# Optimization experiments

Hardware: AMD Instinct MI355X
Metric: run time of the kernel (lower is better)

The kernel has to match this reference:

```python
import jax, jax.numpy as jnp
import numpy as np

B = 64          # batch of graphs
N_GOALS = 16
N_SHELVES = 112
N = N_GOALS + N_SHELVES   # 128 nodes per graph
L = 5           # num_layers
D = 32          # node_embedding_dim
DE = 32         # edge_embedding_dim
DT = 32         # timestep_embedding_dim
D_MSG_IN = 2 * D + DT + 1  # 97


def setup_inputs() -> dict:
    key = jax.random.key(0)
    ks = iter(jax.random.split(key, 40))
    def nrm(shape, s=0.05):
        return jax.random.normal(next(ks), shape, jnp.float32) * s
    inp = {}
    inp["pos"] = jax.random.uniform(next(ks), (B, N_SHELVES, 2), jnp.float32, -1.0, 1.0)
    inp["timesteps"] = jax.random.randint(next(ks), (B,), 0, 1000)
    inp["goal_pos"] = jax.random.uniform(next(ks), (N_GOALS, 2), jnp.float32, -1.0, 1.0)
    inp["W_hin"] = nrm((2, D));            inp["b_hin"] = nrm((D,))
    inp["W_msg1"] = nrm((L, D_MSG_IN, DE)); inp["b_msg1"] = nrm((L, DE))
    inp["W_msg2"] = nrm((L, DE, DE));       inp["b_msg2"] = nrm((L, DE))
    inp["W_att"] = nrm((L, DE, 1));         inp["b_att"] = nrm((L, 1))
    inp["W_pos1"] = nrm((L, DE, DE));       inp["b_pos1"] = nrm((L, DE))
    inp["W_pos2"] = nrm((L, DE, 1));        inp["b_pos2"] = nrm((L, 1))
    inp["W_node1"] = nrm((L - 1, DE + D, D)); inp["b_node1"] = nrm((L - 1, D))
    inp["W_node2"] = nrm((L - 1, D, D));      inp["b_node2"] = nrm((L - 1, D))
    inp["W_t"] = nrm((L - 1, DT, DT));        inp["b_t"] = nrm((L - 1, DT))
    return inp


def _forward(pos, timesteps, goal_pos, W_hin, b_hin, W_msg1, b_msg1, W_msg2, b_msg2,
             W_att, b_att, W_pos1, b_pos1, W_pos2, b_pos2,
             W_node1, b_node1, W_node2, b_node2, W_t, b_t):
    silu = jax.nn.silu
    b = pos.shape[0]
    n_g = goal_pos.shape[0]
    n_sh = pos.shape[1]
    n = n_g + n_sh
    num_layers = W_msg1.shape[0]

    # fully-connected edge template per graph (PyG: edge_index[0]=src=row, edge_index[1]=dst=col)
    src_l = jnp.repeat(jnp.arange(n), n)
    dst_l = jnp.tile(jnp.arange(n), n)
    offs = (jnp.arange(b) * n)[:, None]
    src = (offs + src_l[None, :]).reshape(-1)   # [b*n*n]
    dst = (offs + dst_l[None, :]).reshape(-1)
    e_batch = jnp.repeat(jnp.arange(b), n * n)  # batch[edge_index[0]]

    # node one-hot features: goals [1,0], shelves [0,1]
    h0 = jnp.concatenate([
        jnp.tile(jnp.array([1.0, 0.0], jnp.float32), (n_g, 1)),
        jnp.tile(jnp.array([0.0, 1.0], jnp.float32), (n_sh, 1)),
    ], axis=0)                                   # [n, 2]
    x = jnp.tile(h0, (b, 1))                     # [b*n, 2]

    # node positions: goal positions (shared template) then shelf positions
    p = jnp.concatenate([jnp.broadcast_to(goal_pos, (b, n_g, 2)), pos], axis=1).reshape(-1, 2)

    # sinusoidal timestep embedding
    dt = b_t.shape[-1]
    half = dt // 2
    freqs = jnp.exp(-jnp.log(10000.0) * jnp.arange(half, dtype=jnp.float32) / half)
    ang = timesteps.astype(jnp.float32)[:, None] * freqs[None, :]
    temb = jnp.concatenate([jnp.cos(ang), jnp.sin(ang)], axis=-1)  # [b, dt]

    h = x @ W_hin + b_hin  # [b*n, D]

    for i in range(num_layers):
        te = temb[e_batch]                       # [E, dt]
        pd = p[dst] - p[src]                     # pos_i - pos_j
        radial = jnp.sum(pd * pd, axis=-1, keepdims=True)
        pd = pd / (jax.lax.stop_gradient(jnp.sqrt(radial)) + 1e-6)
        m = jnp.concatenate([h[dst], h[src], radial, te], axis=-1)  # [E, 97]
        m = silu(m @ W_msg1[i] + b_msg1[i])
        m = silu(m @ W_msg2[i] + b_msg2[i])
        m = m * jax.nn.sigmoid(m @ W_att[i] + b_att[i])             # attention gate
        pw = silu(m @ W_pos1[i] + b_pos1[i]) @ W_pos2[i] + b_pos2[i]  # [E, 1]
        aggr_h = jax.ops.segment_sum(m, dst, num_segments=b * n)    # scatter-add
        # scatter-mean: every node receives exactly n incoming edges (fully connected incl. self-loop)
        aggr_p = jax.ops.segment_sum(pd * pw, dst, num_segments=b * n) / n
        if i < num_layers - 1:
            u = silu(jnp.concatenate([h, aggr_h], axis=-1) @ W_node1[i] + b_node1[i])
            u = u @ W_node2[i] + b_node2[i]
            h = jnp.where(u > 0, u, 0.01 * u) + h   # LeakyReLU + residual
            temb = silu(temb @ W_t[i] + b_t[i])
        p = aggr_p + p

    return p.reshape(b, n, 2)[:, n_g:, :].reshape(pos.shape)


def reference(pos, timesteps, goal_pos, W_hin, b_hin, W_msg1, b_msg1, W_msg2, b_msg2,
              W_att, b_att, W_pos1, b_pos1, W_pos2, b_pos2,
              W_node1, b_node1, W_node2, b_node2, W_t, b_t):
    return _forward(pos, timesteps, goal_pos, W_hin, b_hin, W_msg1, b_msg1, W_msg2, b_msg2,
                    W_att, b_att, W_pos1, b_pos1, W_pos2, b_pos2,
                    W_node1, b_node1, W_node2, b_node2, W_t, b_t)
```

## Files before the change

### kernel.cpp

```cpp
#include <hip/hip_runtime.h>
#include <hip/hip_bf16.h>

constexpr int B = 64;
constexpr int NG = 16;
constexpr int NSH = 112;
constexpr int N = 128;
constexpr int NN = B * N;
constexpr int L = 5;

constexpr int OFF_H     = 0;
constexpr int OFF_P0    = OFF_H + NN * 32;
constexpr int OFF_P1    = OFF_P0 + NN * 2;
constexpr int OFF_TEMB0 = OFF_P1 + NN * 2;
constexpr int OFF_TEMB1 = OFF_TEMB0 + B * 32;
constexpr int OFF_HA0   = OFF_TEMB1 + B * 32;
constexpr int OFF_HA1   = OFF_HA0 + NN * 32;
constexpr int OFF_HB0   = OFF_HA1 + NN * 32;
constexpr int OFF_HB1   = OFF_HB0 + NN * 16;

typedef __attribute__((ext_vector_type(8))) short bf16x8;
typedef __attribute__((ext_vector_type(4))) float f32x4;

__device__ __forceinline__ float fsigmoid(float x) {
    return __builtin_amdgcn_rcpf(1.0f + __expf(-x));
}
__device__ __forceinline__ float fsilu(float x) { return x * fsigmoid(x); }
__device__ __forceinline__ short f2bfs(float f) {
    union { __hip_bfloat16 b; short s; } u; u.b = __float2bfloat16(f); return u.s;
}
__device__ __forceinline__ float bf2f(unsigned short u) {
    union { unsigned int i; float f; } v; v.i = ((unsigned int)u) << 16; return v.f;
}
__device__ __forceinline__ unsigned int pk_trunc(float lo, float hi) {
    union { float f; unsigned int u; } a, b;
    a.f = hi; b.f = lo;
    return __builtin_amdgcn_perm(a.u, b.u, 0x07060302u);
}

__global__ __launch_bounds__(256) void setup_pre_kernel(
    float* __restrict__ ws,
    const float* __restrict__ pos, const int* __restrict__ tsteps,
    const float* __restrict__ goal_pos,
    const float* __restrict__ W_hin, const float* __restrict__ b_hin,
    const float* __restrict__ W_msg1, const float* __restrict__ b_msg1)
{
    __shared__ float sT[32];
    const int t = threadIdx.x, bx = blockIdx.x;
    const int tid = bx * 256 + t;
    const int c = tid & 31, node = tid >> 5, g = node >> 7, local = node & 127;
    const int row = (local < NG) ? 0 : 1;

    if (t < 32) {
        const float tf = (float)tsteps[g];
        const int jj = (t < 16) ? t : (t - 16);
        const float ang = tf * expf(-logf(10000.0f) * (float)jj / 16.0f);
        sT[t] = (t < 16) ? cosf(ang) : sinf(ang);
    }
    __syncthreads();
    if ((bx & 15) == 0 && t < 32) ws[OFF_TEMB0 + g * 32 + t] = sT[t];

    ws[OFF_H + tid] = W_hin[row * 32 + c] + b_hin[c];

    if (tid < NN * 2) {
        const int d = tid & 1, nd = tid >> 1, g0 = nd >> 7, loc = nd & 127;
        ws[OFF_P0 + tid] = (loc < NG) ? goal_pos[loc * 2 + d]
                                      : pos[(g0 * NSH + (loc - NG)) * 2 + d];
    }

    const float* __restrict__ W1 = W_msg1;
    float accA = b_msg1[c], accB = 0.f;
#pragma unroll
    for (int k = 0; k < 32; ++k) {
        const float hk = W_hin[row * 32 + k] + b_hin[k];
        accA += hk * W1[k * 32 + c];
        accB += hk * W1[(32 + k) * 32 + c];
    }
#pragma unroll
    for (int k = 0; k < 32; ++k)
        accA += sT[k] * W1[(65 + k) * 32 + c];
    ws[OFF_HA0 + tid] = accA;
    ((unsigned short*)(ws + OFF_HB0))[tid] = (unsigned short)f2bfs(accB);
}

__global__ __attribute__((amdgpu_flat_work_group_size(256, 256)))
__attribute__((amdgpu_waves_per_eu(2, 4))) void edge_kernel(
    float* __restrict__ ws,
    const float* __restrict__ W_msg1, const float* __restrict__ b_msg1,
    const float* __restrict__ W_msg2, const float* __restrict__ b_msg2,
    const float* __restrict__ W_att, const float* __restrict__ b_att,
    const float* __restrict__ W_pos1, const float* __restrict__ b_pos1,
    const float* __restrict__ W_pos2, const float* __restrict__ b_pos2,
    const float* __restrict__ W_node1, const float* __restrict__ b_node1,
    const float* __restrict__ W_node2, const float* __restrict__ b_node2,
    const float* __restrict__ W_t, const float* __restrict__ b_t,
    float* __restrict__ out, int l)
{
    __shared__ unsigned short sHBh[128 * 40];
    __shared__ float sPx[128], sPy[128];
    __shared__ __align__(16) unsigned char uraw[14336];
    __shared__ float sAgg[16][36];
    __shared__ float2 sAgp[16];

    unsigned int* mbuf = (unsigned int*)uraw;
    float2* spn = (float2*)(uraw + 10240);
    float (*sH)[36] = (float(*)[36])uraw;
    unsigned int* nmb = (unsigned int*)(uraw + 2304);

    const int t = threadIdx.x;
    const int bx = blockIdx.x;
    const int g = bx >> 4, qp = bx & 15;
    const int gbase = g << 7;
    const int par = l & 1, op = (l + 1) & 1;

    const float* __restrict__ HAin = ws + (par ? OFF_HA1 : OFF_HA0);
    const unsigned short* __restrict__ HBin = (const unsigned short*)(ws + (par ? OFF_HB1 : OFF_HB0));
    const float* __restrict__ Pin = ws + (par ? OFF_P1 : OFF_P0);

#pragma unroll
    for (int ch = 0; ch < 2; ++ch) {
        const int chunk = t + (ch << 8);
        const int row = chunk >> 2, g4 = chunk & 3;
        *(uint4*)(sHBh + row * 40 + (g4 << 3)) =
            *(const uint4*)(HBin + (gbase + row) * 32 + (g4 << 3));
    }
    if (t < 128) {
        sPx[t] = Pin[(gbase + t) * 2];
        sPy[t] = Pin[(gbase + t) * 2 + 1];
    }
    __syncthreads();

    const int lane = t & 63, w = t >> 6;
    const int c = lane & 15, rg = lane >> 4, kk = rg << 3;

    const float* __restrict__ Wm2L = W_msg2 + l * 1024;
    const float* __restrict__ Wp1L = W_pos1 + l * 1024;
    bf16x8 WB1c0, WB1c1, WBpc0, WBpc1, WBac;
#pragma unroll
    for (int j = 0; j < 8; ++j) {
        WB1c0[j] = f2bfs(Wm2L[(kk + j) * 32 + c]);
        WB1c1[j] = f2bfs(Wm2L[(kk + j) * 32 + c + 16]);
        const int pk = ((kk + j) & 1) * 16 + ((kk + j) >> 1);
        WBpc0[j] = f2bfs(Wp1L[pk * 32 + c]);
        WBpc1[j] = f2bfs(Wp1L[pk * 32 + c + 16]);
        WBac[j]  = f2bfs(W_att[l * 32 + pk]);
    }
    float vwr[8];
    {
        const float* wrR = W_msg1 + l * 97 * 32 + 64 * 32 + kk;
#pragma unroll
        for (int j = 0; j < 8; ++j) vwr[j] = wrR[j];
    }
    const float batt  = b_att[l];
    const float vbm20 = b_msg2[l * 32 + c], vbm21 = b_msg2[l * 32 + c + 16];
    const float vbp10 = b_pos1[l * 32 + c], vbp11 = b_pos1[l * 32 + c + 16];
    const float vwp20 = W_pos2[l * 32 + c], vwp21 = W_pos2[l * 32 + c + 16];
    const float bp2   = b_pos2[l];

    unsigned int* mbA = mbuf + w * 320;
    unsigned int* mbB = mbuf + (w + 4) * 320;

    const int dlA = w, dlB = w + 4;
    const int dlocA = (qp << 3) + dlA, dlocB = (qp << 3) + dlB;
    float vhaA[8], vhaB[8];
    {
        const float* haRA = HAin + (gbase + dlocA) * 32 + kk;
        const float* haRB = HAin + (gbase + dlocB) * 32 + kk;
#pragma unroll
        for (int j = 0; j < 8; ++j) { vhaA[j] = haRA[j]; vhaB[j] = haRB[j]; }
    }
    const float pxdA = sPx[dlocA], pydA = sPy[dlocA];
    const float pxdB = sPx[dlocB], pydB = sPy[dlocB];

    float aghc0A = 0.f, aghc1A = 0.f, apxA = 0.f, apyA = 0.f, spnxA = 0.f, spnyA = 0.f;
    float aghc0B = 0.f, aghc1B = 0.f, apxB = 0.f, apyB = 0.f, spnxB = 0.f, spnyB = 0.f;

#pragma unroll 1
    for (int half = 0; half < 2; ++half) {
        const int src = (half << 6) + lane;
        const float sx = sPx[src], sy = sPy[src];
        const float dxA = pxdA - sx, dyA = pydA - sy;
        const float dxB = pxdB - sx, dyB = pydB - sy;
        const float radialA = dxA * dxA + dyA * dyA;
        const float radialB = dxB * dxB + dyB * dyB;
        const float invA = __builtin_amdgcn_rcpf(__builtin_amdgcn_sqrtf(radialA) + 1e-6f);
        const float invB = __builtin_amdgcn_rcpf(__builtin_amdgcn_sqrtf(radialB) + 1e-6f);
        const float pnxA = dxA * invA, pnyA = dyA * invA;
        const float pnxB = dxB * invB, pnyB = dyB * invB;
        spnxA += pnxA; spnyA += pnyA;
        spnxB += pnxB; spnyB += pnyB;
        spn[w * 64 + lane]       = (float2){pnxA, pnyA};
        spn[(w + 4) * 64 + lane] = (float2){pnxB, pnyB};

#pragma unroll
        for (int tt = 0; tt < 4; ++tt) {
            const float rad_tA = __shfl(radialA, c + (tt << 4));
            const float rad_tB = __shfl(radialB, c + (tt << 4));
            uint4 hraw = *(const uint4*)(sHBh + ((half << 6) + c + (tt << 4)) * 40 + kk);
            const unsigned short* hs = (const unsigned short*)&hraw;
            float xA[8], xB[8];
#pragma unroll
            for (int j = 0; j < 8; ++j) {
                const float hb = bf2f(hs[j]);
                xA[j] = fsilu(vhaA[j] + hb + rad_tA * vwr[j]);
                xB[j] = fsilu(vhaB[j] + hb + rad_tB * vwr[j]);
            }
            union { unsigned int u[4]; bf16x8 v; } afA, afB;
#pragma unroll
            for (int d = 0; d < 4; ++d) {
                afA.u[d] = pk_trunc(xA[2 * d], xA[2 * d + 1]);
                afB.u[d] = pk_trunc(xB[2 * d], xB[2 * d + 1]);
            }
            f32x4 a0A = (f32x4){vbm20, vbm20, vbm20, vbm20};
            f32x4 a1A = (f32x4){vbm21, vbm21, vbm21, vbm21};
            f32x4 a0B = a0A, a1B = a1A;
            a0A = __builtin_amdgcn_mfma_f32_16x16x32_bf16(afA.v, WB1c0, a0A, 0, 0, 0);
            a1A = __builtin_amdgcn_mfma_f32_16x16x32_bf16(afA.v, WB1c1, a1A, 0, 0, 0);
            a0B = __builtin_amdgcn_mfma_f32_16x16x32_bf16(afB.v, WB1c0, a0B, 0, 0, 0);
            a1B = __builtin_amdgcn_mfma_f32_16x16x32_bf16(afB.v, WB1c1, a1B, 0, 0, 0);

            float s0A[4], s1A[4], s0B[4], s1B[4];
#pragma unroll
            for (int j = 0; j < 4; ++j) {
                s0A[j] = fsilu(a0A[j]);
                s1A[j] = fsilu(a1A[j]);
                s0B[j] = fsilu(a0B[j]);
                s1B[j] = fsilu(a1B[j]);
                mbA[((rg << 2) + j) * 20 + c] = pk_trunc(s0A[j], s1A[j]);
                mbB[((rg << 2) + j) * 20 + c] = pk_trunc(s0B[j], s1B[j]);
            }

            union { uint4 u; bf16x8 v; } qaA, qaB;
            qaA.u = *(const uint4*)(mbA + c * 20 + (rg << 2));
            qaB.u = *(const uint4*)(mbB + c * 20 + (rg << 2));
            f32x4 zaA = (f32x4){batt, batt, batt, batt};
            f32x4 zaB = zaA;
            f32x4 z0A = (f32x4){0.f, 0.f, 0.f, 0.f};
            f32x4 z1A = z0A, z0B = z0A, z1B = z0A;
            zaA = __builtin_amdgcn_mfma_f32_16x16x32_bf16(qaA.v, WBac,  zaA, 0, 0, 0);
            z0A = __builtin_amdgcn_mfma_f32_16x16x32_bf16(qaA.v, WBpc0, z0A, 0, 0, 0);
            z1A = __builtin_amdgcn_mfma_f32_16x16x32_bf16(qaA.v, WBpc1, z1A, 0, 0, 0);
            zaB = __builtin_amdgcn_mfma_f32_16x16x32_bf16(qaB.v, WBac,  zaB, 0, 0, 0);
            z0B = __builtin_amdgcn_mfma_f32_16x16x32_bf16(qaB.v, WBpc0, z0B, 0, 0, 0);
            z1B = __builtin_amdgcn_mfma_f32_16x16x32_bf16(qaB.v, WBpc1, z1B, 0, 0, 0);
#pragma unroll
            for (int j = 0; j < 4; ++j) {
                const float attA = fsigmoid(zaA[j]);
                const float attB = fsigmoid(zaB[j]);
                aghc0A += attA * s0A[j];
                aghc1A += attA * s1A[j];
                aghc0B += attB * s0B[j];
                aghc1B += attB * s1B[j];
                const float q0A = fsilu(attA * z0A[j] + vbp10);
                const float q1A = fsilu(attA * z1A[j] + vbp11);
                const float q0B = fsilu(attB * z0B[j] + vbp10);
                const float q1B = fsilu(attB * z1B[j] + vbp11);
                const float pwpA = q0A * vwp20 + q1A * vwp21;
                const float pwpB = q0B * vwp20 + q1B * vwp21;
                const float2 pnA = spn[w * 64 + (tt << 4) + (rg << 2) + j];
                const float2 pnB = spn[(w + 4) * 64 + (tt << 4) + (rg << 2) + j];
                apxA += pwpA * pnA.x;
                apyA += pwpA * pnA.y;
                apxB += pwpB * pnB.x;
                apyB += pwpB * pnB.y;
            }
        }
    }

    aghc0A += __shfl_xor(aghc0A, 16); aghc0A += __shfl_xor(aghc0A, 32);
    aghc1A += __shfl_xor(aghc1A, 16); aghc1A += __shfl_xor(aghc1A, 32);
    aghc0B += __shfl_xor(aghc0B, 16); aghc0B += __shfl_xor(aghc0B, 32);
    aghc1B += __shfl_xor(aghc1B, 16); aghc1B += __shfl_xor(aghc1B, 32);
#pragma unroll
    for (int off = 1; off < 64; off <<= 1) {
        apxA  += __shfl_xor(apxA, off);
        apyA  += __shfl_xor(apyA, off);
        spnxA += __shfl_xor(spnxA, off);
        spnyA += __shfl_xor(spnyA, off);
        apxB  += __shfl_xor(apxB, off);
        apyB  += __shfl_xor(apyB, off);
        spnxB += __shfl_xor(spnxB, off);
        spnyB += __shfl_xor(spnyB, off);
    }
    if (l < L - 1) {
        if (lane < 32) {
            sAgg[dlA][lane] = (lane < 16) ? aghc0A : aghc1A;
            sAgg[dlB][lane] = (lane < 16) ? aghc0B : aghc1B;
        }
        if (lane == 0) {
            sAgp[dlA] = (float2){(apxA + bp2 * spnxA) * (1.0f / 128.0f),
                                 (apyA + bp2 * spnyA) * (1.0f / 128.0f)};
            sAgp[dlB] = (float2){(apxB + bp2 * spnxB) * (1.0f / 128.0f),
                                 (apyB + bp2 * spnyB) * (1.0f / 128.0f)};
        }
    } else if (lane == 0) {
        if (dlocA >= NG) {
            out[(g * NSH + (dlocA - NG)) * 2]     = pxdA + (apxA + bp2 * spnxA) * (1.0f / 128.0f);
            out[(g * NSH + (dlocA - NG)) * 2 + 1] = pydA + (apyA + bp2 * spnyA) * (1.0f / 128.0f);
        }
        if (dlocB >= NG) {
            out[(g * NSH + (dlocB - NG)) * 2]     = pxdB + (apxB + bp2 * spnxB) * (1.0f / 128.0f);
            out[(g * NSH + (dlocB - NG)) * 2 + 1] = pydB + (apyB + bp2 * spnyB) * (1.0f / 128.0f);
        }
    }
    if (l == L - 1) return;

    __syncthreads();

    if (t < 64) {
        const int nbase = bx << 3;
        float* __restrict__ HAout = ws + (op ? OFF_HA1 : OFF_HA0);
        unsigned short* __restrict__ HBout = (unsigned short*)(ws + (op ? OFF_HB1 : OFF_HB0));
        float* __restrict__ Pout = ws + (op ? OFF_P1 : OFF_P0);

        {
            const int row8 = lane >> 3, seg = lane & 7;
            const float* hsrc = ws + OFF_H + (nbase + row8) * 32 + (seg << 2);
#pragma unroll
            for (int j = 0; j < 4; ++j) sH[row8][(seg << 2) + j] = hsrc[j];
        }

        const float* __restrict__ Wn1 = W_node1 + l * 2048;
        const float* __restrict__ Wn2 = W_node2 + l * 1024;
        const float* __restrict__ W1  = W_msg1 + (l + 1) * 97 * 32;
        bf16x8 B1[2][2], B2[2], Ba[2], Bb[2];
#pragma unroll
        for (int j = 0; j < 8; ++j) {
            const int pk = ((kk + j) & 1) * 16 + ((kk + j) >> 1);
#pragma unroll
            for (int nh = 0; nh < 2; ++nh) {
                B1[0][nh][j] = f2bfs(Wn1[(kk + j) * 32 + nh * 16 + c]);
                B1[1][nh][j] = f2bfs(Wn1[(32 + kk + j) * 32 + nh * 16 + c]);
                B2[nh][j]    = f2bfs(Wn2[pk * 32 + nh * 16 + c]);
                Ba[nh][j]    = f2bfs(W1[pk * 32 + nh * 16 + c]);
                Bb[nh][j]    = f2bfs(W1[(32 + pk) * 32 + nh * 16 + c]);
            }
        }

        const int c2 = lane & 31;
        const float* __restrict__ tin = ws + (par ? OFF_TEMB1 : OFF_TEMB0) + g * 32;
        const float* __restrict__ Wt = W_t + l * 1024;
        float a2 = b_t[l * 32 + c2];
#pragma unroll
        for (int k = 0; k < 32; ++k) a2 += tin[k] * Wt[k * 32 + c2];
        const float tnew = fsilu(a2);
        float tv = b_msg1[(l + 1) * 32 + c2];
#pragma unroll
        for (int k = 0; k < 32; ++k) tv += __shfl(tnew, k) * W1[(65 + k) * 32 + c2];
        if ((bx & 15) == 0 && lane < 32)
            ws[(par ? OFF_TEMB0 : OFF_TEMB1) + g * 32 + lane] = tnew;

        union { unsigned int u[4]; bf16x8 v; } A0, A1;
#pragma unroll
        for (int d = 0; d < 4; ++d) {
            A0.u[d] = pk_trunc(sH[c][kk + 2 * d],   sH[c][kk + 2 * d + 1]);
            A1.u[d] = pk_trunc(sAgg[c][kk + 2 * d], sAgg[c][kk + 2 * d + 1]);
        }
        f32x4 u1[2];
#pragma unroll
        for (int nh = 0; nh < 2; ++nh) {
            const float bb = b_node1[l * 32 + nh * 16 + c];
            f32x4 acc = (f32x4){bb, bb, bb, bb};
            acc = __builtin_amdgcn_mfma_f32_16x16x32_bf16(A0.v, B1[0][nh], acc, 0, 0, 0);
            acc = __builtin_amdgcn_mfma_f32_16x16x32_bf16(A1.v, B1[1][nh], acc, 0, 0, 0);
            u1[nh] = acc;
        }

#pragma unroll
        for (int j = 0; j < 4; ++j)
            nmb[((rg << 2) + j) * 20 + c] = pk_trunc(fsilu(u1[0][j]), fsilu(u1[1][j]));
        union { uint4 q; bf16x8 v; } qa;
        qa.q = *(const uint4*)(nmb + c * 20 + (rg << 2));
        f32x4 u2[2];
#pragma unroll
        for (int nh = 0; nh < 2; ++nh) {
            const float bb = b_node2[l * 32 + nh * 16 + c];
            f32x4 acc = (f32x4){bb, bb, bb, bb};
            u2[nh] = __builtin_amdgcn_mfma_f32_16x16x32_bf16(qa.v, B2[nh], acc, 0, 0, 0);
        }

        float hp0[4], hp1[4];
#pragma unroll
        for (int j = 0; j < 4; ++j) {
            const int row = (rg << 2) + j;
            const float h0 = sH[row][c], h1 = sH[row][c + 16];
            const float v0 = u2[0][j], v1 = u2[1][j];
            hp0[j] = (v0 > 0.f ? v0 : 0.01f * v0) + h0;
            hp1[j] = (v1 > 0.f ? v1 : 0.01f * v1) + h1;
            if (row < 8) {
                ws[OFF_H + (nbase + row) * 32 + c]      = hp0[j];
                ws[OFF_H + (nbase + row) * 32 + c + 16] = hp1[j];
            }
            nmb[row * 20 + c] = pk_trunc(hp0[j], hp1[j]);
        }

        qa.q = *(const uint4*)(nmb + c * 20 + (rg << 2));
        f32x4 ha[2], hb[2];
        {
            f32x4 zz = (f32x4){0.f, 0.f, 0.f, 0.f};
#pragma unroll
            for (int nh = 0; nh < 2; ++nh) {
                ha[nh] = __builtin_amdgcn_mfma_f32_16x16x32_bf16(qa.v, Ba[nh], zz, 0, 0, 0);
                hb[nh] = __builtin_amdgcn_mfma_f32_16x16x32_bf16(qa.v, Bb[nh], zz, 0, 0, 0);
            }
        }
        const float tv0 = __shfl(tv, c), tv1 = __shfl(tv, c + 16);
#pragma unroll
        for (int j = 0; j < 4; ++j) {
            const int row = (rg << 2) + j;
            if (row < 8) {
                const int node = nbase + row;
                HAout[node * 32 + c]      = ha[0][j] + tv0;
                HAout[node * 32 + c + 16] = ha[1][j] + tv1;
                HBout[node * 32 + c]      = (unsigned short)f2bfs(hb[0][j]);
                HBout[node * 32 + c + 16] = (unsigned short)f2bfs(hb[1][j]);
            }
        }

        if (lane < 16) {
            const int dl2 = lane >> 1, d = lane & 1;
            const int node = nbase + dl2;
            const float ag = d ? sAgp[dl2].y : sAgp[dl2].x;
            Pout[node * 2 + d] = (par ? ws[OFF_P1 + node * 2 + d]
                                      : ws[OFF_P0 + node * 2 + d]) + ag;
        }
    }
}

extern "C" void kernel_launch(void* const* d_in, const int* in_sizes, int n_in,
                              void* d_out, int out_size, void* d_ws, size_t ws_size,
                              hipStream_t stream)
{
    const float* pos      = (const float*)d_in[0];
    const int*   tsteps   = (const int*)d_in[1];
    const float* goal_pos = (const float*)d_in[2];
    const float* W_hin    = (const float*)d_in[3];
    const float* b_hin    = (const float*)d_in[4];
    const float* W_msg1   = (const float*)d_in[5];
    const float* b_msg1   = (const float*)d_in[6];
    const float* W_msg2   = (const float*)d_in[7];
    const float* b_msg2   = (const float*)d_in[8];
    const float* W_att    = (const float*)d_in[9];
    const float* b_att    = (const float*)d_in[10];
    const float* W_pos1   = (const float*)d_in[11];
    const float* b_pos1   = (const float*)d_in[12];
    const float* W_pos2   = (const float*)d_in[13];
    const float* b_pos2   = (const float*)d_in[14];
    const float* W_node1  = (const float*)d_in[15];
    const float* b_node1  = (const float*)d_in[16];
    const float* W_node2  = (const float*)d_in[17];
    const float* b_node2  = (const float*)d_in[18];
    const float* W_t      = (const float*)d_in[19];
    const float* b_t      = (const float*)d_in[20];

    float* ws = (float*)d_ws;

    setup_pre_kernel<<<1024, 256, 0, stream>>>(ws, pos, tsteps, goal_pos,
                                               W_hin, b_hin, W_msg1, b_msg1);

    for (int l = 0; l < L; ++l)
        edge_kernel<<<1024, 256, 0, stream>>>(ws, W_msg1, b_msg1, W_msg2, b_msg2,
                                              W_att, b_att, W_pos1, b_pos1,
                                              W_pos2, b_pos2, W_node1, b_node1,
                                              W_node2, b_node2, W_t, b_t,
                                              (float*)d_out, l);
}
```

Before: 290.2 us.

## Fuse all message-passing layers into one cooperative persistent kernel with grid sync

Replaces the five per-layer edge_kernel launches with a single cooperative kernel that loops over layers and uses grid.sync between them. Each block handles 16 or 32 destination nodes of one graph instead of the previous 1024-block split. The node update for the next layer is fused into the same block. This removes launch overhead and inter-kernel gaps. In exchange the grid shrinks to 512 or 256 blocks and relies on grid-wide barriers, which may lower parallelism and add barrier cost.

```diff
diff --git a/kernel.cpp b/kernel.cpp
--- a/kernel.cpp
+++ b/kernel.cpp
@@ -1,5 +1,8 @@
 #include <hip/hip_runtime.h>
 #include <hip/hip_bf16.h>
+#include <hip/hip_cooperative_groups.h>
+
+namespace cg = cooperative_groups;
 
 constexpr int B = 64;
 constexpr int NG = 16;
@@ -80,6 +83,367 @@
         accA += sT[k] * W1[(65 + k) * 32 + c];
     ws[OFF_HA0 + tid] = accA;
     ((unsigned short*)(ws + OFF_HB0))[tid] = (unsigned short)f2bfs(accB);
+}
+
+template <int NQP>
+__global__ __attribute__((amdgpu_flat_work_group_size(256, 256)))
+__attribute__((amdgpu_waves_per_eu(2, 4))) void fused_layers_kernel(
+    float* __restrict__ ws,
+    const float* __restrict__ W_msg1, const float* __restrict__ b_msg1,
+    const float* __restrict__ W_msg2, const float* __restrict__ b_msg2,
+    const float* __restrict__ W_att, const float* __restrict__ b_att,
+    const float* __restrict__ W_pos1, const float* __restrict__ b_pos1,
+    const float* __restrict__ W_pos2, const float* __restrict__ b_pos2,
+    const float* __restrict__ W_node1, const float* __restrict__ b_node1,
+    const float* __restrict__ W_node2, const float* __restrict__ b_node2,
+    const float* __restrict__ W_t, const float* __restrict__ b_t,
+    float* __restrict__ out)
+{
+    constexpr int DST  = 128 / NQP;
+    constexpr int SI   = DST / 8;
+    constexpr int BOFF = DST / 2;
+    constexpr int EPP  = DST / 16;
+
+    __shared__ unsigned short sHBh[128 * 40];
+    __shared__ float sPx[128], sPy[128];
+    __shared__ __align__(16) unsigned char uraw[14336];
+    __shared__ float sAgg[32][36];
+    __shared__ float2 sAgp[32];
+
+    unsigned int* mbuf = (unsigned int*)uraw;
+    float2* spn = (float2*)(uraw + 10240);
+    float (*sH)[36] = (float(*)[36])uraw;
+    unsigned int* nmb = (unsigned int*)(uraw + 2304);
+
+    cg::grid_group grid = cg::this_grid();
+
+    const int t = threadIdx.x;
+    const int bx = blockIdx.x;
+    const int g = bx / NQP, qp = bx % NQP;
+    const int gbase = g << 7;
+
+    const int lane = t & 63, w = t >> 6;
+    const int c = lane & 15, rg = lane >> 4, kk = rg << 3;
+
+    unsigned int* mbA = mbuf + w * 320;
+    unsigned int* mbB = mbuf + (w + 4) * 320;
+
+    for (int l = 0; l < L; ++l) {
+        const int par = l & 1, op = par ^ 1;
+
+        const float* __restrict__ HAin = ws + (par ? OFF_HA1 : OFF_HA0);
+        const unsigned short* __restrict__ HBin =
+            (const unsigned short*)(ws + (par ? OFF_HB1 : OFF_HB0));
+        const float* __restrict__ Pin = ws + (par ? OFF_P1 : OFF_P0);
+
+#pragma unroll
+        for (int ch = 0; ch < 2; ++ch) {
+            const int chunk = t + (ch << 8);
+            const int row = chunk >> 2, g4 = chunk & 3;
+            *(uint4*)(sHBh + row * 40 + (g4 << 3)) =
+                *(const uint4*)(HBin + (gbase + row) * 32 + (g4 << 3));
+        }
+        if (t < 128) {
+            sPx[t] = Pin[(gbase + t) * 2];
+            sPy[t] = Pin[(gbase + t) * 2 + 1];
+        }
+        __syncthreads();
+
+        const float* __restrict__ Wm2L = W_msg2 + l * 1024;
+        const float* __restrict__ Wp1L = W_pos1 + l * 1024;
+        bf16x8 WB1c0, WB1c1, WBpc0, WBpc1, WBac;
+#pragma unroll
+        for (int j = 0; j < 8; ++j) {
+            WB1c0[j] = f2bfs(Wm2L[(kk + j) * 32 + c]);
+            WB1c1[j] = f2bfs(Wm2L[(kk + j) * 32 + c + 16]);
+            const int pk = ((kk + j) & 1) * 16 + ((kk + j) >> 1);
+            WBpc0[j] = f2bfs(Wp1L[pk * 32 + c]);
+            WBpc1[j] = f2bfs(Wp1L[pk * 32 + c + 16]);
+            WBac[j]  = f2bfs(W_att[l * 32 + pk]);
+        }
+        float vwr[8];
+        {
+            const float* wrR = W_msg1 + l * 97 * 32 + 64 * 32 + kk;
+#pragma unroll
+            for (int j = 0; j < 8; ++j) vwr[j] = wrR[j];
+        }
+        const float batt  = b_att[l];
+        const float vbm20 = b_msg2[l * 32 + c], vbm21 = b_msg2[l * 32 + c + 16];
+        const float vbp10 = b_pos1[l * 32 + c], vbp11 = b_pos1[l * 32 + c + 16];
+        const float vwp20 = W_pos2[l * 32 + c], vwp21 = W_pos2[l * 32 + c + 16];
+        const float bp2   = b_pos2[l];
+
+#pragma unroll 1
+        for (int si = 0; si < SI; ++si) {
+            const int dlA = (si << 2) + w, dlB = dlA + BOFF;
+            const int dlocA = qp * DST + dlA, dlocB = qp * DST + dlB;
+            float vhaA[8], vhaB[8];
+            {
+                const float* haRA = HAin + (gbase + dlocA) * 32 + kk;
+                const float* haRB = HAin + (gbase + dlocB) * 32 + kk;
+#pragma unroll
+                for (int j = 0; j < 8; ++j) { vhaA[j] = haRA[j]; vhaB[j] = haRB[j]; }
+            }
+            const float pxdA = sPx[dlocA], pydA = sPy[dlocA];
+            const float pxdB = sPx[dlocB], pydB = sPy[dlocB];
+
+            float aghc0A = 0.f, aghc1A = 0.f, apxA = 0.f, apyA = 0.f, spnxA = 0.f, spnyA = 0.f;
+            float aghc0B = 0.f, aghc1B = 0.f, apxB = 0.f, apyB = 0.f, spnxB = 0.f, spnyB = 0.f;
+
+#pragma unroll 1
+            for (int half = 0; half < 2; ++half) {
+                const int src = (half << 6) + lane;
+                const float sx = sPx[src], sy = sPy[src];
+                const float dxA = pxdA - sx, dyA = pydA - sy;
+                const float dxB = pxdB - sx, dyB = pydB - sy;
+                const float radialA = dxA * dxA + dyA * dyA;
+                const float radialB = dxB * dxB + dyB * dyB;
+                const float invA = __builtin_amdgcn_rcpf(__builtin_amdgcn_sqrtf(radialA) + 1e-6f);
+                const float invB = __builtin_amdgcn_rcpf(__builtin_amdgcn_sqrtf(radialB) + 1e-6f);
+                const float pnxA = dxA * invA, pnyA = dyA * invA;
+                const float pnxB = dxB * invB, pnyB = dyB * invB;
+                spnxA += pnxA; spnyA += pnyA;
+                spnxB += pnxB; spnyB += pnyB;
+                spn[w * 64 + lane]       = (float2){pnxA, pnyA};
+                spn[(w + 4) * 64 + lane] = (float2){pnxB, pnyB};
+
+#pragma unroll
+                for (int tt = 0; tt < 4; ++tt) {
+                    const float rad_tA = __shfl(radialA, c + (tt << 4));
+                    const float rad_tB = __shfl(radialB, c + (tt << 4));
+                    uint4 hraw = *(const uint4*)(sHBh + ((half << 6) + c + (tt << 4)) * 40 + kk);
+                    const unsigned short* hs = (const unsigned short*)&hraw;
+                    float xA[8], xB[8];
+#pragma unroll
+                    for (int j = 0; j < 8; ++j) {
+                        const float hb = bf2f(hs[j]);
+                        xA[j] = fsilu(vhaA[j] + hb + rad_tA * vwr[j]);
+                        xB[j] = fsilu(vhaB[j] + hb + rad_tB * vwr[j]);
+                    }
+                    union { unsigned int u[4]; bf16x8 v; } afA, afB;
+#pragma unroll
+                    for (int d = 0; d < 4; ++d) {
+                        afA.u[d] = pk_trunc(xA[2 * d], xA[2 * d + 1]);
+                        afB.u[d] = pk_trunc(xB[2 * d], xB[2 * d + 1]);
+                    }
+                    f32x4 a0A = (f32x4){vbm20, vbm20, vbm20, vbm20};
+                    f32x4 a1A = (f32x4){vbm21, vbm21, vbm21, vbm21};
+                    f32x4 a0B = a0A, a1B = a1A;
+                    a0A = __builtin_amdgcn_mfma_f32_16x16x32_bf16(afA.v, WB1c0, a0A, 0, 0, 0);
+                    a1A = __builtin_amdgcn_mfma_f32_16x16x32_bf16(afA.v, WB1c1, a1A, 0, 0, 0);
+                    a0B = __builtin_amdgcn_mfma_f32_16x16x32_bf16(afB.v, WB1c0, a0B, 0, 0, 0);
+                    a1B = __builtin_amdgcn_mfma_f32_16x16x32_bf16(afB.v, WB1c1, a1B, 0, 0, 0);
+
+                    float s0A[4], s1A[4], s0B[4], s1B[4];
+#pragma unroll
+                    for (int j = 0; j < 4; ++j) {
+                        s0A[j] = fsilu(a0A[j]);
+                        s1A[j] = fsilu(a1A[j]);
+                        s0B[j] = fsilu(a0B[j]);
+                        s1B[j] = fsilu(a1B[j]);
+                        mbA[((rg << 2) + j) * 20 + c] = pk_trunc(s0A[j], s1A[j]);
+                        mbB[((rg << 2) + j) * 20 + c] = pk_trunc(s0B[j], s1B[j]);
+                    }
+
+                    union { uint4 u; bf16x8 v; } qaA, qaB;
+                    qaA.u = *(const uint4*)(mbA + c * 20 + (rg << 2));
+                    qaB.u = *(const uint4*)(mbB + c * 20 + (rg << 2));
+                    f32x4 zaA = (f32x4){batt, batt, batt, batt};
+                    f32x4 zaB = zaA;
+                    f32x4 z0A = (f32x4){0.f, 0.f, 0.f, 0.f};
+                    f32x4 z1A = z0A, z0B = z0A, z1B = z0A;
+                    zaA = __builtin_amdgcn_mfma_f32_16x16x32_bf16(qaA.v, WBac,  zaA, 0, 0, 0);
+                    z0A = __builtin_amdgcn_mfma_f32_16x16x32_bf16(qaA.v, WBpc0, z0A, 0, 0, 0);
+                    z1A = __builtin_amdgcn_mfma_f32_16x16x32_bf16(qaA.v, WBpc1, z1A, 0, 0, 0);
+                    zaB = __builtin_amdgcn_mfma_f32_16x16x32_bf16(qaB.v, WBac,  zaB, 0, 0, 0);
+                    z0B = __builtin_amdgcn_mfma_f32_16x16x32_bf16(qaB.v, WBpc0, z0B, 0, 0, 0);
+                    z1B = __builtin_amdgcn_mfma_f32_16x16x32_bf16(qaB.v, WBpc1, z1B, 0, 0, 0);
+#pragma unroll
+                    for (int j = 0; j < 4; ++j) {
+                        const float attA = fsigmoid(zaA[j]);
+                        const float attB = fsigmoid(zaB[j]);
+                        aghc0A += attA * s0A[j];
+                        aghc1A += attA * s1A[j];
+                        aghc0B += attB * s0B[j];
+                        aghc1B += attB * s1B[j];
+                        const float q0A = fsilu(attA * z0A[j] + vbp10);
+                        const float q1A = fsilu(attA * z1A[j] + vbp11);
+                        const float q0B = fsilu(attB * z0B[j] + vbp10);
+                        const float q1B = fsilu(attB * z1B[j] + vbp11);
+                        const float pwpA = q0A * vwp20 + q1A * vwp21;
+                        const float pwpB = q0B * vwp20 + q1B * vwp21;
+                        const float2 pnA = spn[w * 64 + (tt << 4) + (rg << 2) + j];
+                        const float2 pnB = spn[(w + 4) * 64 + (tt << 4) + (rg << 2) + j];
+                        apxA += pwpA * pnA.x;
+                        apyA += pwpA * pnA.y;
+                        apxB += pwpB * pnB.x;
+                        apyB += pwpB * pnB.y;
+                    }
+                }
+            }
+
+            aghc0A += __shfl_xor(aghc0A, 16); aghc0A += __shfl_xor(aghc0A, 32);
+            aghc1A += __shfl_xor(aghc1A, 16); aghc1A += __shfl_xor(aghc1A, 32);
+            aghc0B += __shfl_xor(aghc0B, 16); aghc0B += __shfl_xor(aghc0B, 32);
+            aghc1B += __shfl_xor(aghc1B, 16); aghc1B += __shfl_xor(aghc1B, 32);
+#pragma unroll
+            for (int off = 1; off < 64; off <<= 1) {
+                apxA  += __shfl_xor(apxA, off);
+                apyA  += __shfl_xor(apyA, off);
+                spnxA += __shfl_xor(spnxA, off);
+                spnyA += __shfl_xor(spnyA, off);
+                apxB  += __shfl_xor(apxB, off);
+                apyB  += __shfl_xor(apyB, off);
+                spnxB += __shfl_xor(spnxB, off);
+                spnyB += __shfl_xor(spnyB, off);
+            }
+            if (l < L - 1) {
+                if (lane < 32) {
+                    sAgg[dlA][lane] = (lane < 16) ? aghc0A : aghc1A;
+                    sAgg[dlB][lane] = (lane < 16) ? aghc0B : aghc1B;
+                }
+                if (lane == 0) {
+                    sAgp[dlA] = (float2){(apxA + bp2 * spnxA) * (1.0f / 128.0f),
+                                         (apyA + bp2 * spnyA) * (1.0f / 128.0f)};
+                    sAgp[dlB] = (float2){(apxB + bp2 * spnxB) * (1.0f / 128.0f),
+                                         (apyB + bp2 * spnyB) * (1.0f / 128.0f)};
+                }
+            } else if (lane == 0) {
+                if (dlocA >= NG) {
+                    out[(g * NSH + (dlocA - NG)) * 2]     = pxdA + (apxA + bp2 * spnxA) * (1.0f / 128.0f);
+                    out[(g * NSH + (dlocA - NG)) * 2 + 1] = pydA + (apyA + bp2 * spnyA) * (1.0f / 128.0f);
+                }
+                if (dlocB >= NG) {
+                    out[(g * NSH + (dlocB - NG)) * 2]     = pxdB + (apxB + bp2 * spnxB) * (1.0f / 128.0f);
+                    out[(g * NSH + (dlocB - NG)) * 2 + 1] = pydB + (apyB + bp2 * spnyB) * (1.0f / 128.0f);
+                }
+            }
+        }
+        if (l == L - 1) break;
+
+        __syncthreads();
+
+        if (t < 64) {
+            float* __restrict__ HAout = ws + (op ? OFF_HA1 : OFF_HA0);
+            unsigned short* __restrict__ HBout = (unsigned short*)(ws + (op ? OFF_HB1 : OFF_HB0));
+            float* __restrict__ Pout = ws + (op ? OFF_P1 : OFF_P0);
+
+            const float* __restrict__ Wn1 = W_node1 + l * 2048;
+            const float* __restrict__ Wn2 = W_node2 + l * 1024;
+            const float* __restrict__ W1n = W_msg1 + (l + 1) * 97 * 32;
+            bf16x8 B1[2][2], B2[2], Ba[2], Bb[2];
+#pragma unroll
+            for (int j = 0; j < 8; ++j) {
+                const int pk = ((kk + j) & 1) * 16 + ((kk + j) >> 1);
+#pragma unroll
+                for (int nh = 0; nh < 2; ++nh) {
+                    B1[0][nh][j] = f2bfs(Wn1[(kk + j) * 32 + nh * 16 + c]);
+                    B1[1][nh][j] = f2bfs(Wn1[(32 + kk + j) * 32 + nh * 16 + c]);
+                    B2[nh][j]    = f2bfs(Wn2[pk * 32 + nh * 16 + c]);
+                    Ba[nh][j]    = f2bfs(W1n[pk * 32 + nh * 16 + c]);
+                    Bb[nh][j]    = f2bfs(W1n[(32 + pk) * 32 + nh * 16 + c]);
+                }
+            }
+
+            const int c2 = lane & 31;
+            const float* __restrict__ tin = ws + (par ? OFF_TEMB1 : OFF_TEMB0) + g * 32;
+            const float* __restrict__ Wt = W_t + l * 1024;
+            float a2 = b_t[l * 32 + c2];
+#pragma unroll
+            for (int k = 0; k < 32; ++k) a2 += tin[k] * Wt[k * 32 + c2];
+            const float tnew = fsilu(a2);
+            float tv = b_msg1[(l + 1) * 32 + c2];
+#pragma unroll
+            for (int k = 0; k < 32; ++k) tv += __shfl(tnew, k) * W1n[(65 + k) * 32 + c2];
+            if (qp == 0 && lane < 32)
+                ws[(par ? OFF_TEMB0 : OFF_TEMB1) + g * 32 + lane] = tnew;
+            const float tv0 = __shfl(tv, c), tv1 = __shfl(tv, c + 16);
+
+#pragma unroll 1
+            for (int ep = 0; ep < EPP; ++ep) {
+                const int nbase = bx * DST + (ep << 4);
+
+                {
+                    const int row = lane >> 2, seg = lane & 3;
+                    const float* hsrc = ws + OFF_H + (nbase + row) * 32 + (seg << 3);
+#pragma unroll
+                    for (int j = 0; j < 8; ++j) sH[row][(seg << 3) + j] = hsrc[j];
+                }
+
+                union { unsigned int u[4]; bf16x8 v; } A0, A1;
+#pragma unroll
+                for (int d = 0; d < 4; ++d) {
+                    A0.u[d] = pk_trunc(sH[c][kk + 2 * d], sH[c][kk + 2 * d + 1]);
+                    A1.u[d] = pk_trunc(sAgg[(ep << 4) + c][kk + 2 * d],
+                                       sAgg[(ep << 4) + c][kk + 2 * d + 1]);
+                }
+                f32x4 u1[2];
+#pragma unroll
+                for (int nh = 0; nh < 2; ++nh) {
+                    const float bb = b_node1[l * 32 + nh * 16 + c];
+                    f32x4 acc = (f32x4){bb, bb, bb, bb};
+                    acc = __builtin_amdgcn_mfma_f32_16x16x32_bf16(A0.v, B1[0][nh], acc, 0, 0, 0);
+                    acc = __builtin_amdgcn_mfma_f32_16x16x32_bf16(A1.v, B1[1][nh], acc, 0, 0, 0);
+                    u1[nh] = acc;
+                }
+
+#pragma unroll
+                for (int j = 0; j < 4; ++j)
+                    nmb[((rg << 2) + j) * 20 + c] = pk_trunc(fsilu(u1[0][j]), fsilu(u1[1][j]));
+                union { uint4 q; bf16x8 v; } qa;
+                qa.q = *(const uint4*)(nmb + c * 20 + (rg << 2));
+                f32x4 u2[2];
+#pragma unroll
+                for (int nh = 0; nh < 2; ++nh) {
+                    const float bb = b_node2[l * 32 + nh * 16 + c];
+                    f32x4 acc = (f32x4){bb, bb, bb, bb};
+                    u2[nh] = __builtin_amdgcn_mfma_f32_16x16x32_bf16(qa.v, B2[nh], acc, 0, 0, 0);
+                }
+
+                float hp0[4], hp1[4];
+#pragma unroll
+                for (int j = 0; j < 4; ++j) {
+                    const int row = (rg << 2) + j;
+                    const float h0 = sH[row][c], h1 = sH[row][c + 16];
+                    const float v0 = u2[0][j], v1 = u2[1][j];
+                    hp0[j] = (v0 > 0.f ? v0 : 0.01f * v0) + h0;
+                    hp1[j] = (v1 > 0.f ? v1 : 0.01f * v1) + h1;
+                    ws[OFF_H + (nbase + row) * 32 + c]      = hp0[j];
+                    ws[OFF_H + (nbase + row) * 32 + c + 16] = hp1[j];
+                    nmb[row * 20 + c] = pk_trunc(hp0[j], hp1[j]);
+                }
+
+                qa.q = *(const uint4*)(nmb + c * 20 + (rg << 2));
+                f32x4 ha[2], hb[2];
+                {
+                    f32x4 zz = (f32x4){0.f, 0.f, 0.f, 0.f};
+#pragma unroll
+                    for (int nh = 0; nh < 2; ++nh) {
+                        ha[nh] = __builtin_amdgcn_mfma_f32_16x16x32_bf16(qa.v, Ba[nh], zz, 0, 0, 0);
+                        hb[nh] = __builtin_amdgcn_mfma_f32_16x16x32_bf16(qa.v, Bb[nh], zz, 0, 0, 0);
+                    }
+                }
+#pragma unroll
+                for (int j = 0; j < 4; ++j) {
+                    const int node = nbase + (rg << 2) + j;
+                    HAout[node * 32 + c]      = ha[0][j] + tv0;
+                    HAout[node * 32 + c + 16] = ha[1][j] + tv1;
+                    HBout[node * 32 + c]      = (unsigned short)f2bfs(hb[0][j]);
+                    HBout[node * 32 + c + 16] = (unsigned short)f2bfs(hb[1][j]);
+                }
+
+                if (lane < 32) {
+                    const int dl2 = lane >> 1, d = lane & 1;
+                    const int node = nbase + dl2;
+                    const float ag = d ? sAgp[(ep << 4) + dl2].y : sAgp[(ep << 4) + dl2].x;
+                    Pout[node * 2 + d] = (par ? ws[OFF_P1 + node * 2 + d]
+                                              : ws[OFF_P0 + node * 2 + d]) + ag;
+                }
+            }
+        }
+
+        grid.sync();
+    }
 }
 
 __global__ __attribute__((amdgpu_flat_work_group_size(256, 256)))
@@ -452,15 +816,43 @@
     const float* W_t      = (const float*)d_in[19];
     const float* b_t      = (const float*)d_in[20];
 
-    float* ws = (float*)d_ws;
+    float* ws   = (float*)d_ws;
+    float* outp = (float*)d_out;
 
     setup_pre_kernel<<<1024, 256, 0, stream>>>(ws, pos, tsteps, goal_pos,
                                                W_hin, b_hin, W_msg1, b_msg1);
 
-    for (int l = 0; l < L; ++l)
-        edge_kernel<<<1024, 256, 0, stream>>>(ws, W_msg1, b_msg1, W_msg2, b_msg2,
-                                              W_att, b_att, W_pos1, b_pos1,
-                                              W_pos2, b_pos2, W_node1, b_node1,
-                                              W_node2, b_node2, W_t, b_t,
-                                              (float*)d_out, l);
+    void* args[] = {
+        (void*)&ws,
+        (void*)&W_msg1, (void*)&b_msg1, (void*)&W_msg2, (void*)&b_msg2,
+        (void*)&W_att,  (void*)&b_att,  (void*)&W_pos1, (void*)&b_pos1,
+        (void*)&W_pos2, (void*)&b_pos2, (void*)&W_node1,(void*)&b_node1,
+        (void*)&W_node2,(void*)&b_node2,(void*)&W_t,    (void*)&b_t,
+        (void*)&outp
+    };
+
+    bool launched = false;
+
+    int maxb8 = 0;
+    if (hipOccupancyMaxActiveBlocksPerMultiprocessor(&maxb8, fused_layers_kernel<8>,
+                                                     256, 0) == hipSuccess && maxb8 >= 2) {
+        launched = hipLaunchCooperativeKernel(fused_layers_kernel<8>, dim3(512), dim3(256),
+                                              args, 0, stream) == hipSuccess;
+    }
+    if (!launched) {
+        int maxb4 = 0;
+        if (hipOccupancyMaxActiveBlocksPerMultiprocessor(&maxb4, fused_layers_kernel<4>,
+                                                         256, 0) == hipSuccess && maxb4 >= 1) {
+            launched = hipLaunchCooperativeKernel(fused_layers_kernel<4>, dim3(256), dim3(256),
+                                                  args, 0, stream) == hipSuccess;
+        }
+    }
+    if (!launched) {
+        for (int l = 0; l < L; ++l)
+            edge_kernel<<<1024, 256, 0, stream>>>(ws, W_msg1, b_msg1, W_msg2, b_msg2,
+                                                  W_att, b_att, W_pos1, b_pos1,
+                                                  W_pos2, b_pos2, W_node1, b_node1,
+                                                  W_node2, b_node2, W_t, b_t,
+                                                  outp, l);
+    }
 }
```

Result: slower. 511.4 us (+76.2%).
